# Performance work log

Measured on AMD Instinct MI355X. Metric: run time of the kernel, lower is better.

## Reference

```python
import jax, jax.numpy as jnp
import numpy as np
import math

B, N, OBS, ACT = 128, 64, 128, 16
D = OBS + ACT          # obs_act_input_dim = 144
DK = 128               # obs_act_output_dim (d_k)
ENC = 128              # encoder_output_dim
FIN = 1                # final_output_dim


def setup_inputs() -> dict:
    key = jax.random.key(0)
    ks = jax.random.split(key, 8)
    s = 0.05
    return {
        "observations": jax.random.normal(ks[0], (B, N, OBS), jnp.float32),
        "policies": jax.random.uniform(ks[1], (B, N, ACT), jnp.float32),
        "actions": jax.random.uniform(ks[2], (B, N, ACT), jnp.float32),
        # torch nn.Linear weights are [out, in]
        "Wk": jax.random.normal(ks[3], (DK, D), jnp.float32) * s,
        "Wq": jax.random.normal(ks[4], (DK, D), jnp.float32) * s,
        "Wv": jax.random.normal(ks[5], (DK, D), jnp.float32) * s,
        "Wenc": jax.random.normal(ks[6], (ENC, OBS), jnp.float32) * s,
        "Wfin": jax.random.normal(ks[7], (FIN, ENC + DK), jnp.float32) * s,
    }


def reference(observations, policies, actions, Wk, Wq, Wv, Wenc, Wfin):
    b, n = observations.shape[0], observations.shape[1]
    d_k = Wk.shape[0]
    oa = jnp.concatenate([observations, actions], axis=-1)      # [B,N,D]
    op = jnp.concatenate([observations, policies], axis=-1)     # [B,N,D]
    k = oa @ Wk.T                                               # [B,N,dk]
    q = oa @ Wq.T                                               # [B,N,dk]
    # torch: bmm(q, k^T).transpose(1,2) -> scores[b,i,j] = q[b,j] . k[b,i]
    scores = jnp.einsum('bjd,bid->bij', q, k)
    w = jax.nn.sigmoid(scores / math.sqrt(d_k))                 # [B,N,N]
    Va = oa @ Wv.T                                              # [B,N,dk] value of obs||action
    Vp = op @ Wv.T                                              # [B,N,dk] value of obs||policy
    # original 5D masked combine reduces to: agg[b,i,m] = (sum_j w[b,i,j]*Va[b,j]
    #   + w[b,i,m]*(Vp[b,m]-Va[b,m])) / N  (policy substituted only where j==m)
    S = jnp.einsum('bij,bjd->bid', w, Va)                       # [B,N,dk]
    agg = (S[:, :, None, :] + w[..., None] * (Vp - Va)[:, None, :, :]) / n  # [B,N,N,dk]
    enc = observations @ Wenc.T                                 # [B,N,ENC]
    enc_rep = jnp.broadcast_to(enc[:, :, None, :], (b, n, n, enc.shape[-1]))
    node = jnp.concatenate([enc_rep, agg], axis=-1)             # [B,N,N,ENC+dk]
    value = node @ Wfin.T                                       # [B,N,N,1]
    weights5 = jnp.broadcast_to(w[:, :, None, :, None], (b, n, n, n, 1))
    return value, weights5
```

## Files before the change

### kernel.cpp

```cpp
#include <hip/hip_runtime.h>
#include <stdint.h>


#define BB 128
#define NN 64
#define OBSD 128
#define ACTD 16
#define DD 144
#define DKD 128
#define RS 168

typedef float f32x4 __attribute__((ext_vector_type(4)));
typedef short bf16x8 __attribute__((ext_vector_type(8)));

#define F_U 16384
#define F_G (F_U + 256)

__device__ __forceinline__ unsigned short bf1(float x) {
  unsigned u = __float_as_uint(x);
  return (unsigned short)((u + 0x7fffu + ((u >> 16) & 1u)) >> 16);
}
__device__ __forceinline__ unsigned int pack_bf2(float x, float y) {
  return (unsigned)bf1(x) | ((unsigned)bf1(y) << 16);
}
__device__ __forceinline__ float bf2f(unsigned short s) {
  return __uint_as_float(((unsigned)s) << 16);
}

__global__ __launch_bounds__(256) void critic_setup(
    const float* __restrict__ Wk, const float* __restrict__ Wq,
    const float* __restrict__ Wv, const float* __restrict__ Wenc,
    const float* __restrict__ Wfin, float* __restrict__ ws)
{
  const int bid = blockIdx.x, t = threadIdx.x;
  if (bid < DD) {
    const int e = bid;
    if (t < 160) {
      float acc = 0.f;
      if (t < DD) {
        float a0=0.f,a1=0.f,a2=0.f,a3=0.f;
        for (int c = 0; c < DKD; c += 4) {
          a0 += Wk[(c+0)*DD + t] * Wq[(c+0)*DD + e];
          a1 += Wk[(c+1)*DD + t] * Wq[(c+1)*DD + e];
          a2 += Wk[(c+2)*DD + t] * Wq[(c+2)*DD + e];
          a3 += Wk[(c+3)*DD + t] * Wq[(c+3)*DD + e];
        }
        acc = (a0+a1)+(a2+a3);
      }
      ((unsigned short*)ws)[e * 160 + t] = bf1(acc);
    }
  } else if (bid == DD) {
    if (t < DD) {
      float a0=0.f,a1=0.f,a2=0.f,a3=0.f;
      for (int c = 0; c < DKD; c += 4) {
        a0 += Wv[(c+0)*DD + t] * Wfin[OBSD + c + 0];
        a1 += Wv[(c+1)*DD + t] * Wfin[OBSD + c + 1];
        a2 += Wv[(c+2)*DD + t] * Wfin[OBSD + c + 2];
        a3 += Wv[(c+3)*DD + t] * Wfin[OBSD + c + 3];
      }
      ws[F_U + t] = (a0+a1)+(a2+a3);
    }
  } else {
    if (t < OBSD) {
      float a0=0.f,a1=0.f,a2=0.f,a3=0.f;
      for (int c = 0; c < 128; c += 4) {
        a0 += Wenc[(c+0)*OBSD + t] * Wfin[c + 0];
        a1 += Wenc[(c+1)*OBSD + t] * Wfin[c + 1];
        a2 += Wenc[(c+2)*OBSD + t] * Wfin[c + 2];
        a3 += Wenc[(c+3)*OBSD + t] * Wfin[c + 3];
      }
      ws[F_G + t] = (a0+a1)+(a2+a3);
    }
  }
}

__global__ __launch_bounds__(512, 2) void critic_fused(
    const float* __restrict__ obs, const float* __restrict__ pol,
    const float* __restrict__ act, const float* __restrict__ ws,
    float* __restrict__ out)
{
  __shared__ __align__(16) unsigned short s_oa[NN * RS];
  __shared__ __align__(16) unsigned short s_T[16 * RS];
  __shared__ __align__(16) float s_w[16 * 68];
  __shared__ unsigned short s_dpa[NN * ACTD];
  __shared__ float s_u[DD];
  __shared__ float s_g[OBSD];
  __shared__ float s_vas[NN], s_dv[NN], s_ve[16], s_sv[16];

  const int tid = threadIdx.x;
  const int b = blockIdx.x >> 2;
  const int i0 = (blockIdx.x & 3) * 16;
  const int wv = tid >> 6, lane = tid & 63;
  const int m = lane & 15, q = lane >> 4;
  const unsigned short* mt = (const unsigned short*)ws;

  {
    const float4* obs4 = (const float4*)(obs + (size_t)b * NN * OBSD);
    for (int idx = tid; idx < 2048; idx += 512) {
      float4 v = obs4[idx];
      int row = idx >> 5, c4 = (idx & 31) * 4;
      *(uint2*)&s_oa[row * RS + c4] = make_uint2(pack_bf2(v.x, v.y), pack_bf2(v.z, v.w));
    }
    if (tid < 256) {
      const float4* act4 = (const float4*)(act + (size_t)b * NN * ACTD);
      const float4* pol4 = (const float4*)(pol + (size_t)b * NN * ACTD);
      float4 a = act4[tid], pp = pol4[tid];
      int row = tid >> 2, t0 = (tid & 3) * 4;
      *(uint2*)&s_oa[row * RS + OBSD + t0] = make_uint2(pack_bf2(a.x, a.y), pack_bf2(a.z, a.w));
      *(uint2*)&s_dpa[row * ACTD + t0] =
          make_uint2(pack_bf2(pp.x - a.x, pp.y - a.y), pack_bf2(pp.z - a.z, pp.w - a.w));
    } else if (tid < 512) {
      int idx = tid - 256;
      int row = idx >> 2, c4 = DD + (idx & 3) * 4;
      *(uint2*)&s_oa[row * RS + c4] = make_uint2(0u, 0u);
    }
    if (tid < DD)             s_u[tid] = ws[F_U + tid];
    else if (tid < DD + OBSD) s_g[tid - DD] = ws[F_G + (tid - DD)];
  }
  __syncthreads();

  f32x4 accT = (f32x4){0.f, 0.f, 0.f, 0.f};
  f32x4 accT8 = (f32x4){0.f, 0.f, 0.f, 0.f};
  #pragma unroll
  for (int ks = 0; ks < 5; ++ks) {
    const int koff = ks * 32 + q * 8;
    bf16x8 a = *(const bf16x8*)&s_oa[(i0 + m) * RS + koff];
    bf16x8 bb = *(const bf16x8*)&mt[(wv * 16 + m) * 160 + koff];
    accT = __builtin_amdgcn_mfma_f32_16x16x32_bf16(a, bb, accT, 0, 0, 0);
    if (wv == 0) {
      bf16x8 b8 = *(const bf16x8*)&mt[(128 + m) * 160 + koff];
      accT8 = __builtin_amdgcn_mfma_f32_16x16x32_bf16(a, b8, accT8, 0, 0, 0);
    }
  }
  #pragma unroll
  for (int r = 0; r < 4; ++r)
    s_T[(q * 4 + r) * RS + wv * 16 + m] = bf1(accT[r]);
  if (wv == 0)
    #pragma unroll
    for (int r = 0; r < 4; ++r)
      s_T[(q * 4 + r) * RS + 128 + m] = bf1(accT8[r]);
  if (tid < 32) {
    int row = tid >> 1, h = tid & 1;
    *(uint4*)&s_T[row * RS + DD + h * 8] = make_uint4(0u, 0u, 0u, 0u);
  }
  __syncthreads();

  if (wv < 4) {
    f32x4 sc = (f32x4){0.f, 0.f, 0.f, 0.f};
    #pragma unroll
    for (int ks = 0; ks < 5; ++ks) {
      const int koff = ks * 32 + q * 8;
      bf16x8 a = *(const bf16x8*)&s_T[m * RS + koff];
      bf16x8 bb = *(const bf16x8*)&s_oa[(wv * 16 + m) * RS + koff];
      sc = __builtin_amdgcn_mfma_f32_16x16x32_bf16(a, bb, sc, 0, 0, 0);
    }
    const float kk = 0.08838834764831845f;
    #pragma unroll
    for (int r = 0; r < 4; ++r)
      s_w[(q * 4 + r) * 68 + wv * 16 + m] = 1.0f / (1.0f + __expf(-sc[r] * kk));
  } else if (wv == 4) {
    float a = 0.f;
    #pragma unroll
    for (int t = 0; t < ACTD; ++t) a += bf2f(s_dpa[lane * ACTD + t]) * s_u[OBSD + t];
    s_dv[lane] = a;
  } else if (wv == 5) {
    float a = 0.f;
    for (int d = 0; d < DD; ++d) a += bf2f(s_oa[lane * RS + d]) * s_u[d];
    s_vas[lane] = a;
  } else if (wv == 6 && lane < 16) {
    float a = 0.f;
    for (int d = 0; d < OBSD; ++d) a += bf2f(s_oa[(i0 + lane) * RS + d]) * s_g[d];
    s_ve[lane] = a;
  }
  __syncthreads();

  if (tid < 16) {
    float a = 0.f;
    for (int j = 0; j < NN; ++j) a += s_w[tid * 68 + j] * s_vas[j];
    s_sv[tid] = a;
  }
  __syncthreads();

  if (tid < 256) {
    const int r = tid >> 4, m4 = (tid & 15) * 4;
    float4 v;
    v.x = s_ve[r] + (s_sv[r] + s_w[r * 68 + m4 + 0] * s_dv[m4 + 0]) * (1.0f / 64.0f);
    v.y = s_ve[r] + (s_sv[r] + s_w[r * 68 + m4 + 1] * s_dv[m4 + 1]) * (1.0f / 64.0f);
    v.z = s_ve[r] + (s_sv[r] + s_w[r * 68 + m4 + 2] * s_dv[m4 + 2]) * (1.0f / 64.0f);
    v.w = s_ve[r] + (s_sv[r] + s_w[r * 68 + m4 + 3] * s_dv[m4 + 3]) * (1.0f / 64.0f);
    *(float4*)(out + ((size_t)(b * 64 + i0 + r) * 64 + m4)) = v;
  }

  float* w5 = out + (size_t)BB * NN * NN;
  #pragma unroll 4
  for (int r = 0; r < 16; ++r) {
    const float4 wv4 = *(const float4*)&s_w[r * 68 + (tid & 15) * 4];
    float4* p4 = (float4*)(w5 + ((size_t)(b * 64 + i0 + r) << 12));
    p4[tid]       = wv4;
    p4[tid + 512] = wv4;
  }
}

extern "C" void kernel_launch(void* const* d_in, const int* in_sizes, int n_in,
                              void* d_out, int out_size, void* d_ws, size_t ws_size,
                              hipStream_t stream) {
  (void)in_sizes; (void)n_in; (void)out_size; (void)ws_size;
  const float* obs  = (const float*)d_in[0];
  const float* pol  = (const float*)d_in[1];
  const float* act  = (const float*)d_in[2];
  const float* Wk   = (const float*)d_in[3];
  const float* Wq   = (const float*)d_in[4];
  const float* Wv   = (const float*)d_in[5];
  const float* Wenc = (const float*)d_in[6];
  const float* Wfin = (const float*)d_in[7];
  float* out = (float*)d_out;
  float* ws  = (float*)d_ws;
  hipLaunchKernelGGL(critic_setup, dim3(DD + 2), dim3(256), 0, stream,
                     Wk, Wq, Wv, Wenc, Wfin, ws);
  hipLaunchKernelGGL(critic_fused, dim3(BB * 4), dim3(512), 0, stream,
                     obs, pol, act, ws, out);
}
```

Measured before the change: 166.4 us.

## Replace MFMA tile kernel with scalar two-row-per-block plane kernel

Rewrites the fused kernel so each 256-thread block handles two query rows (4096 blocks) instead of 16 rows per 512-thread block. Bilinear scores now use scalar FP32 dot products against an fp32 Wq^T·Wk matrix read from global memory, replacing bf16 MFMA. Reductions are done with wave shuffles, which removes one barrier stage. The goal is more blocks to spread the dominant weights5 output writes. The cost is that each block reloads the full per-batch observation tile (32x redundant loads) and does the scalar math redundantly.

```diff
diff --git a/kernel.cpp b/kernel.cpp
--- a/kernel.cpp
+++ b/kernel.cpp
@@ -7,14 +7,12 @@
 #define OBSD 128
 #define ACTD 16
 #define DD 144
-#define DKD 128
-#define RS 168
+#define RSW 146
 
 typedef float f32x4 __attribute__((ext_vector_type(4)));
-typedef short bf16x8 __attribute__((ext_vector_type(8)));
-
-#define F_U 16384
-#define F_G (F_U + 256)
+
+#define U_OFF 20736
+#define G_OFF 20880
 
 __device__ __forceinline__ unsigned short bf1(float x) {
   unsigned u = __float_as_uint(x);
@@ -34,31 +32,27 @@
 {
   const int bid = blockIdx.x, t = threadIdx.x;
   if (bid < DD) {
-    const int e = bid;
-    if (t < 160) {
-      float acc = 0.f;
-      if (t < DD) {
-        float a0=0.f,a1=0.f,a2=0.f,a3=0.f;
-        for (int c = 0; c < DKD; c += 4) {
-          a0 += Wk[(c+0)*DD + t] * Wq[(c+0)*DD + e];
-          a1 += Wk[(c+1)*DD + t] * Wq[(c+1)*DD + e];
-          a2 += Wk[(c+2)*DD + t] * Wq[(c+2)*DD + e];
-          a3 += Wk[(c+3)*DD + t] * Wq[(c+3)*DD + e];
-        }
-        acc = (a0+a1)+(a2+a3);
+    const int d = bid;
+    if (t < DD) {
+      float a0=0.f,a1=0.f,a2=0.f,a3=0.f;
+      for (int c = 0; c < 128; c += 4) {
+        a0 += Wk[(c+0)*DD + d] * Wq[(c+0)*DD + t];
+        a1 += Wk[(c+1)*DD + d] * Wq[(c+1)*DD + t];
+        a2 += Wk[(c+2)*DD + d] * Wq[(c+2)*DD + t];
+        a3 += Wk[(c+3)*DD + d] * Wq[(c+3)*DD + t];
       }
-      ((unsigned short*)ws)[e * 160 + t] = bf1(acc);
+      ws[d * DD + t] = (a0+a1)+(a2+a3);
     }
   } else if (bid == DD) {
     if (t < DD) {
       float a0=0.f,a1=0.f,a2=0.f,a3=0.f;
-      for (int c = 0; c < DKD; c += 4) {
+      for (int c = 0; c < 128; c += 4) {
         a0 += Wv[(c+0)*DD + t] * Wfin[OBSD + c + 0];
         a1 += Wv[(c+1)*DD + t] * Wfin[OBSD + c + 1];
         a2 += Wv[(c+2)*DD + t] * Wfin[OBSD + c + 2];
         a3 += Wv[(c+3)*DD + t] * Wfin[OBSD + c + 3];
       }
-      ws[F_U + t] = (a0+a1)+(a2+a3);
+      ws[U_OFF + t] = (a0+a1)+(a2+a3);
     }
   } else {
     if (t < OBSD) {
@@ -69,135 +63,130 @@
         a2 += Wenc[(c+2)*OBSD + t] * Wfin[c + 2];
         a3 += Wenc[(c+3)*OBSD + t] * Wfin[c + 3];
       }
-      ws[F_G + t] = (a0+a1)+(a2+a3);
-    }
-  }
-}
-
-__global__ __launch_bounds__(512, 2) void critic_fused(
+      ws[G_OFF + t] = (a0+a1)+(a2+a3);
+    }
+  }
+}
+
+__global__ __launch_bounds__(256) void critic_plane(
     const float* __restrict__ obs, const float* __restrict__ pol,
     const float* __restrict__ act, const float* __restrict__ ws,
     float* __restrict__ out)
 {
-  __shared__ __align__(16) unsigned short s_oa[NN * RS];
-  __shared__ __align__(16) unsigned short s_T[16 * RS];
-  __shared__ __align__(16) float s_w[16 * 68];
-  __shared__ unsigned short s_dpa[NN * ACTD];
+  __shared__ __align__(16) unsigned short s_oa[NN * RSW];
+  __shared__ float s_T0[DD], s_T1[DD];
   __shared__ float s_u[DD];
   __shared__ float s_g[OBSD];
-  __shared__ float s_vas[NN], s_dv[NN], s_ve[16], s_sv[16];
-
-  const int tid = threadIdx.x;
-  const int b = blockIdx.x >> 2;
-  const int i0 = (blockIdx.x & 3) * 16;
-  const int wv = tid >> 6, lane = tid & 63;
-  const int m = lane & 15, q = lane >> 4;
-  const unsigned short* mt = (const unsigned short*)ws;
+  __shared__ float s_dv[NN];
+  __shared__ __align__(16) float s_w0[NN], s_w1[NN];
+  __shared__ float s_ve[2];
+
+  const int t = threadIdx.x;
+  const int b = blockIdx.x >> 5;
+  const int i0 = (blockIdx.x & 31) * 2;
 
   {
     const float4* obs4 = (const float4*)(obs + (size_t)b * NN * OBSD);
-    for (int idx = tid; idx < 2048; idx += 512) {
+    #pragma unroll
+    for (int k = 0; k < 8; ++k) {
+      int idx = t + k * 256;
       float4 v = obs4[idx];
       int row = idx >> 5, c4 = (idx & 31) * 4;
-      *(uint2*)&s_oa[row * RS + c4] = make_uint2(pack_bf2(v.x, v.y), pack_bf2(v.z, v.w));
-    }
-    if (tid < 256) {
-      const float4* act4 = (const float4*)(act + (size_t)b * NN * ACTD);
-      const float4* pol4 = (const float4*)(pol + (size_t)b * NN * ACTD);
-      float4 a = act4[tid], pp = pol4[tid];
-      int row = tid >> 2, t0 = (tid & 3) * 4;
-      *(uint2*)&s_oa[row * RS + OBSD + t0] = make_uint2(pack_bf2(a.x, a.y), pack_bf2(a.z, a.w));
-      *(uint2*)&s_dpa[row * ACTD + t0] =
-          make_uint2(pack_bf2(pp.x - a.x, pp.y - a.y), pack_bf2(pp.z - a.z, pp.w - a.w));
-    } else if (tid < 512) {
-      int idx = tid - 256;
-      int row = idx >> 2, c4 = DD + (idx & 3) * 4;
-      *(uint2*)&s_oa[row * RS + c4] = make_uint2(0u, 0u);
-    }
-    if (tid < DD)             s_u[tid] = ws[F_U + tid];
-    else if (tid < DD + OBSD) s_g[tid - DD] = ws[F_G + (tid - DD)];
+      unsigned* p = (unsigned*)&s_oa[row * RSW + c4];
+      p[0] = pack_bf2(v.x, v.y);
+      p[1] = pack_bf2(v.z, v.w);
+    }
+    const float4* act4 = (const float4*)(act + (size_t)b * NN * ACTD);
+    float4 a = act4[t];
+    int row = t >> 2, t0 = (t & 3) * 4;
+    unsigned* p = (unsigned*)&s_oa[row * RSW + OBSD + t0];
+    p[0] = pack_bf2(a.x, a.y);
+    p[1] = pack_bf2(a.z, a.w);
+    for (int idx = t; idx < DD + OBSD; idx += 256) {
+      if (idx < DD) s_u[idx] = ws[U_OFF + idx];
+      else          s_g[idx - DD] = ws[G_OFF + (idx - DD)];
+    }
   }
   __syncthreads();
 
-  f32x4 accT = (f32x4){0.f, 0.f, 0.f, 0.f};
-  f32x4 accT8 = (f32x4){0.f, 0.f, 0.f, 0.f};
-  #pragma unroll
-  for (int ks = 0; ks < 5; ++ks) {
-    const int koff = ks * 32 + q * 8;
-    bf16x8 a = *(const bf16x8*)&s_oa[(i0 + m) * RS + koff];
-    bf16x8 bb = *(const bf16x8*)&mt[(wv * 16 + m) * 160 + koff];
-    accT = __builtin_amdgcn_mfma_f32_16x16x32_bf16(a, bb, accT, 0, 0, 0);
-    if (wv == 0) {
-      bf16x8 b8 = *(const bf16x8*)&mt[(128 + m) * 160 + koff];
-      accT8 = __builtin_amdgcn_mfma_f32_16x16x32_bf16(a, b8, accT8, 0, 0, 0);
-    }
-  }
-  #pragma unroll
-  for (int r = 0; r < 4; ++r)
-    s_T[(q * 4 + r) * RS + wv * 16 + m] = bf1(accT[r]);
-  if (wv == 0)
-    #pragma unroll
-    for (int r = 0; r < 4; ++r)
-      s_T[(q * 4 + r) * RS + 128 + m] = bf1(accT8[r]);
-  if (tid < 32) {
-    int row = tid >> 1, h = tid & 1;
-    *(uint4*)&s_T[row * RS + DD + h * 8] = make_uint4(0u, 0u, 0u, 0u);
+  if (t < DD) {
+    float a0 = 0.f, a1 = 0.f;
+    const float* mt = ws + t;
+    for (int d = 0; d < DD; ++d) {
+      float x0 = bf2f(s_oa[i0 * RSW + d]);
+      float x1 = bf2f(s_oa[(i0 + 1) * RSW + d]);
+      float mv = mt[d * DD];
+      a0 += x0 * mv; a1 += x1 * mv;
+    }
+    s_T0[t] = a0; s_T1[t] = a1;
+  } else if (t >= 192) {
+    const int m = t - 192;
+    const float* pr = pol + ((size_t)b * NN + m) * ACTD;
+    const float* ar = act + ((size_t)b * NN + m) * ACTD;
+    float a = 0.f;
+    #pragma unroll
+    for (int k = 0; k < ACTD; ++k) a += (pr[k] - ar[k]) * s_u[OBSD + k];
+    s_dv[m] = a;
   }
   __syncthreads();
 
-  if (wv < 4) {
-    f32x4 sc = (f32x4){0.f, 0.f, 0.f, 0.f};
-    #pragma unroll
-    for (int ks = 0; ks < 5; ++ks) {
-      const int koff = ks * 32 + q * 8;
-      bf16x8 a = *(const bf16x8*)&s_T[m * RS + koff];
-      bf16x8 bb = *(const bf16x8*)&s_oa[(wv * 16 + m) * RS + koff];
-      sc = __builtin_amdgcn_mfma_f32_16x16x32_bf16(a, bb, sc, 0, 0, 0);
+  float sv0 = 0.f, sv1 = 0.f, w0v = 0.f, w1v = 0.f;
+  if (t < 64) {
+    float a0 = 0.f, a1 = 0.f, av = 0.f;
+    for (int e = 0; e < DD; ++e) {
+      float x = bf2f(s_oa[t * RSW + e]);
+      a0 += s_T0[e] * x;
+      a1 += s_T1[e] * x;
+      av += s_u[e] * x;
     }
     const float kk = 0.08838834764831845f;
-    #pragma unroll
-    for (int r = 0; r < 4; ++r)
-      s_w[(q * 4 + r) * 68 + wv * 16 + m] = 1.0f / (1.0f + __expf(-sc[r] * kk));
-  } else if (wv == 4) {
-    float a = 0.f;
-    #pragma unroll
-    for (int t = 0; t < ACTD; ++t) a += bf2f(s_dpa[lane * ACTD + t]) * s_u[OBSD + t];
-    s_dv[lane] = a;
-  } else if (wv == 5) {
-    float a = 0.f;
-    for (int d = 0; d < DD; ++d) a += bf2f(s_oa[lane * RS + d]) * s_u[d];
-    s_vas[lane] = a;
-  } else if (wv == 6 && lane < 16) {
-    float a = 0.f;
-    for (int d = 0; d < OBSD; ++d) a += bf2f(s_oa[(i0 + lane) * RS + d]) * s_g[d];
-    s_ve[lane] = a;
+    w0v = 1.0f / (1.0f + __expf(-a0 * kk));
+    w1v = 1.0f / (1.0f + __expf(-a1 * kk));
+    s_w0[t] = w0v; s_w1[t] = w1v;
+    float p0 = w0v * av, p1 = w1v * av;
+    #pragma unroll
+    for (int off = 32; off; off >>= 1) {
+      p0 += __shfl_xor(p0, off);
+      p1 += __shfl_xor(p1, off);
+    }
+    sv0 = p0; sv1 = p1;
+  } else if (t >= 128 && t < 192) {
+    const int l = t - 128;
+    float p = bf2f(s_oa[i0 * RSW + l]) * s_g[l]
+            + bf2f(s_oa[i0 * RSW + 64 + l]) * s_g[64 + l];
+    #pragma unroll
+    for (int off = 32; off; off >>= 1) p += __shfl_xor(p, off);
+    if (l == 0) s_ve[0] = p;
+  } else if (t >= 192) {
+    const int l = t - 192;
+    float p = bf2f(s_oa[(i0 + 1) * RSW + l]) * s_g[l]
+            + bf2f(s_oa[(i0 + 1) * RSW + 64 + l]) * s_g[64 + l];
+    #pragma unroll
+    for (int off = 32; off; off >>= 1) p += __shfl_xor(p, off);
+    if (l == 0) s_ve[1] = p;
   }
   __syncthreads();
 
-  if (tid < 16) {
-    float a = 0.f;
-    for (int j = 0; j < NN; ++j) a += s_w[tid * 68 + j] * s_vas[j];
-    s_sv[tid] = a;
-  }
-  __syncthreads();
-
-  if (tid < 256) {
-    const int r = tid >> 4, m4 = (tid & 15) * 4;
-    float4 v;
-    v.x = s_ve[r] + (s_sv[r] + s_w[r * 68 + m4 + 0] * s_dv[m4 + 0]) * (1.0f / 64.0f);
-    v.y = s_ve[r] + (s_sv[r] + s_w[r * 68 + m4 + 1] * s_dv[m4 + 1]) * (1.0f / 64.0f);
-    v.z = s_ve[r] + (s_sv[r] + s_w[r * 68 + m4 + 2] * s_dv[m4 + 2]) * (1.0f / 64.0f);
-    v.w = s_ve[r] + (s_sv[r] + s_w[r * 68 + m4 + 3] * s_dv[m4 + 3]) * (1.0f / 64.0f);
-    *(float4*)(out + ((size_t)(b * 64 + i0 + r) * 64 + m4)) = v;
-  }
-
-  float* w5 = out + (size_t)BB * NN * NN;
-  #pragma unroll 4
-  for (int r = 0; r < 16; ++r) {
-    const float4 wv4 = *(const float4*)&s_w[r * 68 + (tid & 15) * 4];
-    float4* p4 = (float4*)(w5 + ((size_t)(b * 64 + i0 + r) << 12));
-    p4[tid]       = wv4;
-    p4[tid + 512] = wv4;
+  if (t < 64) {
+    float* valout = out + ((size_t)(b * NN + i0)) * NN;
+    valout[t]      = s_ve[0] + (sv0 + w0v * s_dv[t]) * 0.015625f;
+    valout[NN + t] = s_ve[1] + (sv1 + w1v * s_dv[t]) * 0.015625f;
+  }
+  {
+    float* w5 = out + (size_t)BB * NN * NN + ((size_t)(b * NN + i0)) * (NN * NN);
+    const int m = t >> 4, j4 = t & 15;
+    const float4 v0 = *(const float4*)&s_w0[j4 * 4];
+    const float4 v1 = *(const float4*)&s_w1[j4 * 4];
+    float4* p0 = (float4*)w5;
+    float4* p1 = (float4*)(w5 + NN * NN);
+    p0[(m +  0) * 16 + j4] = v0;
+    p0[(m + 16) * 16 + j4] = v0;
+    p0[(m + 32) * 16 + j4] = v0;
+    p0[(m + 48) * 16 + j4] = v0;
+    p1[(m +  0) * 16 + j4] = v1;
+    p1[(m + 16) * 16 + j4] = v1;
+    p1[(m + 32) * 16 + j4] = v1;
+    p1[(m + 48) * 16 + j4] = v1;
   }
 }
 
@@ -217,6 +206,6 @@
   float* ws  = (float*)d_ws;
   hipLaunchKernelGGL(critic_setup, dim3(DD + 2), dim3(256), 0, stream,
                      Wk, Wq, Wv, Wenc, Wfin, ws);
-  hipLaunchKernelGGL(critic_fused, dim3(BB * 4), dim3(512), 0, stream,
+  hipLaunchKernelGGL(critic_plane, dim3(4096), dim3(256), 0, stream,
                      obs, pol, act, ws, out);
 }
```

After: 206.7 us. 24.2% more time.
